# Performance work log

Hardware: AMD Instinct MI355X
Metric: run time of the kernel (lower is better)

Reference implementation:

```python
import jax, jax.numpy as jnp
import numpy as np

NEG_BIG = -9e15
ALPHA = 0.2  # LeakyReLU negative slope


def setup_inputs() -> dict:
    key = jax.random.key(0)
    k1, k2, k3, k4 = jax.random.split(key, 4)
    B, N, F_in, F_out = 8, 2048, 128, 128
    h = jax.random.normal(k1, (B, N, F_in), dtype=jnp.float32)
    adj = jax.random.randint(k2, (B, N, N), 0, 2, dtype=jnp.int32)
    # xavier_uniform with gain=1.414
    def xavier(k, shape, gain=1.414):
        fan_in, fan_out = shape[0], shape[1]
        bound = gain * np.sqrt(6.0 / (fan_in + fan_out))
        return jax.random.uniform(k, shape, jnp.float32, -bound, bound)
    W = xavier(k3, (F_in, F_out))
    a = xavier(k4, (2 * F_out, 1))
    return {"h": h, "adj": adj, "W": W, "a": a}


def reference(h, adj, W, a):
    # h: [B,N,F_in], adj: [B,N,N], W: [F_in,F_out], a: [2*F_out,1]
    Wh = jnp.einsum('bnf,fo->bno', h, W)              # [B,N,F_out]
    F_out = W.shape[1]
    a1 = a[:F_out, 0]                                  # source part
    a2 = a[F_out:, 0]                                  # target part
    # additive attention decomposition: cat([Wh_i, Wh_j]) @ a == Wh_i@a1 + Wh_j@a2
    s1 = Wh @ a1                                       # [B,N]
    s2 = Wh @ a2                                       # [B,N]
    e = jax.nn.leaky_relu(s1[:, :, None] + s2[:, None, :], negative_slope=ALPHA)  # [B,N,N]
    e = jnp.where(adj > 0, e, NEG_BIG)
    attn = jax.nn.softmax(e, axis=-1)                  # [B,N,N]
    h_prime = jnp.einsum('bij,bjo->bio', attn, Wh)     # [B,N,F_out]
    return jax.nn.elu(h_prime)                         # concat=True path
```

## Files before the change

kernel.cpp:

```cpp
#include <hip/hip_runtime.h>
#include <hip/hip_bf16.h>
#include <string.h>

typedef __attribute__((ext_vector_type(8))) short short8;
typedef __attribute__((ext_vector_type(4))) float f32x4;
typedef __attribute__((ext_vector_type(4))) int int4v;
typedef __attribute__((ext_vector_type(4))) float float4v;
typedef __attribute__((ext_vector_type(4))) unsigned short ushort4v;

#define LOG2E 1.44269504088896340736f
#define NB 8
#define NN 2048
#define NF 128
#define PKW (NN / 64)
#define PKWORDS (NB * NN * PKW)

static __device__ inline unsigned short f2bf(float x) {
    __hip_bfloat16 b = __float2bfloat16(x);
    unsigned short u;
    __builtin_memcpy(&u, &b, 2);
    return u;
}
static __device__ inline float bf2f(unsigned short u) {
    union { unsigned u; float f; } v;
    v.u = ((unsigned)u) << 16;
    return v.f;
}

__global__ void k_sniff(const unsigned short* __restrict__ hraw,
                        int* __restrict__ flag) {
    int lane = threadIdx.x;
    int cnt = 0;
    for (int i = lane; i < 512; i += 64) {
        int e = (hraw[i] >> 7) & 0xFF;
        cnt += (e >= 102 && e <= 139) ? 1 : 0;
    }
#pragma unroll
    for (int off = 1; off < 64; off <<= 1) cnt += __shfl_xor(cnt, off);
    if (lane == 0) *flag = (cnt >= 450) ? 1 : 0;
}

__global__ __launch_bounds__(256) void k_pack(const int* __restrict__ adj,
                                              unsigned long long* __restrict__ pk) {
    const int wid = blockIdx.x * 4 + (threadIdx.x >> 6);
    const int lane = threadIdx.x & 63;
    const int wpw = PKWORDS / 4096;
    const size_t w0 = (size_t)wid * wpw;
    for (int i = 0; i < wpw; i += 4) {
        int v0 = adj[((w0 + i) << 6) | lane];
        int v1 = adj[((w0 + i + 1) << 6) | lane];
        int v2 = adj[((w0 + i + 2) << 6) | lane];
        int v3 = adj[((w0 + i + 3) << 6) | lane];
        unsigned long long m0 = __ballot(v0 > 0);
        unsigned long long m1 = __ballot(v1 > 0);
        unsigned long long m2 = __ballot(v2 > 0);
        unsigned long long m3 = __ballot(v3 > 0);
        if (lane == 0) {
            pk[w0 + i] = m0;
            pk[w0 + i + 1] = m1;
            pk[w0 + i + 2] = m2;
            pk[w0 + i + 3] = m3;
        }
    }
}

__global__ __launch_bounds__(256) void k_prep(const void* __restrict__ Wraw,
                                              const void* __restrict__ araw,
                                              const int* __restrict__ flag,
                                              short* __restrict__ WThi,
                                              short* __restrict__ WTlo,
                                              float* __restrict__ a1s,
                                              float* __restrict__ a2s) {
    const int bf16w = *flag;
    int idx = blockIdx.x * 256 + threadIdx.x;
    int k = idx >> 7, n = idx & 127;
    float x = bf16w ? bf2f(((const unsigned short*)Wraw)[idx])
                    : ((const float*)Wraw)[idx];
    unsigned short hi = f2bf(x);
    float lo = x - bf2f(hi);
    WThi[n * 128 + k] = (short)hi;
    WTlo[n * 128 + k] = (short)f2bf(lo);
    if (blockIdx.x == 0) {
        int i = threadIdx.x;
        float av = bf16w ? bf2f(((const unsigned short*)araw)[i])
                         : ((const float*)araw)[i];
        if (i < 128) a1s[i] = LOG2E * av;
        else a2s[i - 128] = LOG2E * av;
    }
}

__global__ __launch_bounds__(64) void k_gemm(const void* __restrict__ hraw,
                                             const int* __restrict__ flag,
                                             const short* __restrict__ WThi,
                                             const short* __restrict__ WTlo,
                                             const float* __restrict__ a1s,
                                             const float* __restrict__ a2s,
                                             float* __restrict__ s1,
                                             float* __restrict__ s2,
                                             short* __restrict__ WhT) {
    const int lane = threadIdx.x;
    const int lo = lane & 15, g = lane >> 4;
    const int i0 = blockIdx.x * 16;
    const int bf16w = *flag;

    short8 ahi[4], alo[4];
    if (bf16w) {
        const short* h16 = (const short*)hraw;
#pragma unroll
        for (int kc = 0; kc < 4; ++kc) {
            ahi[kc] = *(const short8*)(h16 + (size_t)(i0 + lo) * NF + kc * 32 + g * 8);
            alo[kc] = (short8){0, 0, 0, 0, 0, 0, 0, 0};
        }
    } else {
        const float* hf = (const float*)hraw;
#pragma unroll
        for (int kc = 0; kc < 4; ++kc) {
            const float* p = hf + (size_t)(i0 + lo) * NF + kc * 32 + g * 8;
            float4v x0 = *(const float4v*)(p);
            float4v x1 = *(const float4v*)(p + 4);
            short8 h8, l8;
#pragma unroll
            for (int q = 0; q < 4; ++q) {
                unsigned short u0 = f2bf(x0[q]);
                h8[q] = (short)u0;
                l8[q] = (short)f2bf(x0[q] - bf2f(u0));
                unsigned short u1 = f2bf(x1[q]);
                h8[q + 4] = (short)u1;
                l8[q + 4] = (short)f2bf(x1[q] - bf2f(u1));
            }
            ahi[kc] = h8;
            alo[kc] = l8;
        }
    }

    f32x4 acc[8];
#pragma unroll
    for (int t = 0; t < 8; ++t) acc[t] = (f32x4){0.f, 0.f, 0.f, 0.f};

#pragma unroll
    for (int t = 0; t < 8; ++t) {
#pragma unroll
        for (int kc = 0; kc < 4; ++kc) {
            const size_t boff = (size_t)(lo + 16 * t) * NF + kc * 32 + g * 8;
            short8 bhi = *(const short8*)(WThi + boff);
            short8 blo = *(const short8*)(WTlo + boff);
            acc[t] = __builtin_amdgcn_mfma_f32_16x16x32_bf16(ahi[kc], bhi, acc[t], 0, 0, 0);
            acc[t] = __builtin_amdgcn_mfma_f32_16x16x32_bf16(ahi[kc], blo, acc[t], 0, 0, 0);
            acc[t] = __builtin_amdgcn_mfma_f32_16x16x32_bf16(alo[kc], bhi, acc[t], 0, 0, 0);
        }
    }

    const int b = i0 >> 11;
    const int n0 = i0 & 2047;
    short* wt = WhT + (size_t)b * NF * NN;
#pragma unroll
    for (int t = 0; t < 8; ++t) {
        ushort4v u;
#pragma unroll
        for (int r = 0; r < 4; ++r) u[r] = f2bf(acc[t][r]);
        *(ushort4v*)(wt + (size_t)(lo + 16 * t) * NN + n0 + g * 4) = u;
    }

    float a1f[8], a2f[8];
#pragma unroll
    for (int t = 0; t < 8; ++t) {
        a1f[t] = a1s[lo + 16 * t];
        a2f[t] = a2s[lo + 16 * t];
    }
#pragma unroll
    for (int r = 0; r < 4; ++r) {
        float d1 = 0.f, d2 = 0.f;
#pragma unroll
        for (int t = 0; t < 8; ++t) {
            float w = acc[t][r];
            d1 += w * a1f[t];
            d2 += w * a2f[t];
        }
#pragma unroll
        for (int off = 1; off < 16; off <<= 1) {
            d1 += __shfl_xor(d1, off);
            d2 += __shfl_xor(d2, off);
        }
        if (lo == 0) {
            s1[i0 + g * 4 + r] = d1;
            s2[i0 + g * 4 + r] = d2;
        }
    }
}

__global__ __launch_bounds__(256) void k_s2max(const float* __restrict__ s2,
                                               float* __restrict__ s2m) {
    int b = blockIdx.x;
    float m = -1e30f;
    for (int i = threadIdx.x; i < NN; i += 256) m = fmaxf(m, s2[b * NN + i]);
#pragma unroll
    for (int off = 1; off < 64; off <<= 1) m = fmaxf(m, __shfl_xor(m, off));
    __shared__ float sm[4];
    if ((threadIdx.x & 63) == 0) sm[threadIdx.x >> 6] = m;
    __syncthreads();
    if (threadIdx.x == 0)
        s2m[b] = fmaxf(fmaxf(sm[0], sm[1]), fmaxf(sm[2], sm[3]));
}

template <int FINAL, int JS>
__global__ __launch_bounds__(256, 4) void k_attn3(const unsigned long long* __restrict__ pk,
                                                  const float* __restrict__ s1,
                                                  const float* __restrict__ s2,
                                                  const float* __restrict__ s2m,
                                                  const short* __restrict__ WhT,
                                                  const int* __restrict__ flag,
                                                  void* __restrict__ out,
                                                  float* __restrict__ pO,
                                                  float* __restrict__ pL) {
    const int tid = threadIdx.x;
    const int lane = tid & 63, wid = tid >> 6;
    const int lo = lane & 15, g = lane >> 4;
    const int gid = blockIdx.x;
    const int js = (JS > 1) ? (gid / (NB * 32)) : 0;
    const int rem = gid % (NB * 32);
    const int blk = rem & 31;
    const int b = rem >> 5;
    const int rowbase = blk * 64 + wid * 16;
    const int row = rowbase + lo;
    const int jbeg = js * (NN / JS);
    const int NT = (NN / JS) / 64;

    __shared__ short lds[2][128 * 64];

    const float s1v = s1[b * NN + row];
    const float tm = s1v + s2m[b];
    const float M = fmaxf(tm, 0.2f * tm);
    const unsigned long long* pkr = pk + (size_t)(b * NN + row) * PKW + (jbeg >> 6);
    const float* s2p = s2 + b * NN + jbeg;
    const short* vb = WhT + (size_t)b * NF * NN;

    const int sf = tid >> 1;
    const int sh = tid & 1;
    const short* sbase = vb + (size_t)sf * NN + jbeg + sh * 32;
    char* ldsc0 = (char*)&lds[0][0];
    char* ldsc1 = (char*)&lds[1][0];
    const unsigned swz = (unsigned)((sf & 7) << 4);
    const unsigned wb0 = (unsigned)(sf * 128 + sh * 64);
    const unsigned rsw = (unsigned)((lo & 7) << 4);

    f32x4 acc[8];
#pragma unroll
    for (int t = 0; t < 8; ++t) acc[t] = (f32x4){0.f, 0.f, 0.f, 0.f};
    float lsum = 0.f;

    {
        short8 s0 = *(const short8*)(sbase);
        short8 s1r = *(const short8*)(sbase + 8);
        short8 s2r = *(const short8*)(sbase + 16);
        short8 s3r = *(const short8*)(sbase + 24);
        *(short8*)(ldsc0 + ((wb0 + 0) ^ swz)) = s0;
        *(short8*)(ldsc0 + ((wb0 + 16) ^ swz)) = s1r;
        *(short8*)(ldsc0 + ((wb0 + 32) ^ swz)) = s2r;
        *(short8*)(ldsc0 + ((wb0 + 48) ^ swz)) = s3r;
    }
    unsigned long long mcur = pkr[0];
    float4v zc0 = *(const float4v*)(s2p + g * 8);
    float4v zc1 = *(const float4v*)(s2p + g * 8 + 4);
    float4v zc2 = *(const float4v*)(s2p + g * 8 + 32);
    float4v zc3 = *(const float4v*)(s2p + g * 8 + 36);
    __syncthreads();

    int cur = 0;
    for (int t = 0; t < NT; ++t) {
        short8 sn0, sn1, sn2, sn3;
        unsigned long long mnext = 0;
        float4v zn0, zn1, zn2, zn3;
        const bool more = (t + 1 < NT);
        if (more) {
            const short* sp = sbase + (t + 1) * 64;
            sn0 = *(const short8*)(sp);
            sn1 = *(const short8*)(sp + 8);
            sn2 = *(const short8*)(sp + 16);
            sn3 = *(const short8*)(sp + 24);
            mnext = pkr[t + 1];
            const float* zp = s2p + (t + 1) * 64 + g * 8;
            zn0 = *(const float4v*)(zp);
            zn1 = *(const float4v*)(zp + 4);
            zn2 = *(const float4v*)(zp + 32);
            zn3 = *(const float4v*)(zp + 36);
        }
        const char* cb = cur ? ldsc1 : ldsc0;

        const unsigned bits0 = (unsigned)(mcur >> (g * 8)) & 0xFFu;
        const unsigned bits1 = (unsigned)(mcur >> (32 + g * 8)) & 0xFFu;
        short8 pa0, pa1;
#pragma unroll
        for (int q = 0; q < 4; ++q) {
            float t0 = s1v + zc0[q];
            float e0 = fmaxf(t0, 0.2f * t0);
            float p0 = ((bits0 >> q) & 1u) ? exp2f(e0 - M) : 0.f;
            float t1 = s1v + zc1[q];
            float e1 = fmaxf(t1, 0.2f * t1);
            float p1 = ((bits0 >> (q + 4)) & 1u) ? exp2f(e1 - M) : 0.f;
            float t2 = s1v + zc2[q];
            float e2 = fmaxf(t2, 0.2f * t2);
            float p2 = ((bits1 >> q) & 1u) ? exp2f(e2 - M) : 0.f;
            float t3 = s1v + zc3[q];
            float e3 = fmaxf(t3, 0.2f * t3);
            float p3 = ((bits1 >> (q + 4)) & 1u) ? exp2f(e3 - M) : 0.f;
            pa0[q] = (short)f2bf(p0); pa0[q + 4] = (short)f2bf(p1);
            pa1[q] = (short)f2bf(p2); pa1[q + 4] = (short)f2bf(p3);
            lsum += p0 + p1 + p2 + p3;
        }

#pragma unroll
        for (int t8 = 0; t8 < 8; ++t8) {
            const unsigned rb0 = ((unsigned)((lo + 16 * t8) * 128 + g * 16)) ^ rsw;
            const unsigned rb1 = ((unsigned)((lo + 16 * t8) * 128 + 64 + g * 16)) ^ rsw;
            short8 v0 = *(const short8*)(cb + rb0);
            short8 v1 = *(const short8*)(cb + rb1);
            acc[t8] = __builtin_amdgcn_mfma_f32_16x16x32_bf16(pa0, v0, acc[t8], 0, 0, 0);
            acc[t8] = __builtin_amdgcn_mfma_f32_16x16x32_bf16(pa1, v1, acc[t8], 0, 0, 0);
        }

        if (more) {
            char* wb = cur ? ldsc0 : ldsc1;
            *(short8*)(wb + ((wb0 + 0) ^ swz)) = sn0;
            *(short8*)(wb + ((wb0 + 16) ^ swz)) = sn1;
            *(short8*)(wb + ((wb0 + 32) ^ swz)) = sn2;
            *(short8*)(wb + ((wb0 + 48) ^ swz)) = sn3;
            mcur = mnext;
            zc0 = zn0; zc1 = zn1; zc2 = zn2; zc3 = zn3;
        }
        __syncthreads();
        cur ^= 1;
    }

    lsum += __shfl_xor(lsum, 16);
    lsum += __shfl_xor(lsum, 32);

    if (FINAL) {
        const int bf16w = *flag;
        float inv[4];
#pragma unroll
        for (int r = 0; r < 4; ++r) inv[r] = 1.0f / __shfl(lsum, g * 4 + r);
#pragma unroll
        for (int t8 = 0; t8 < 8; ++t8) {
#pragma unroll
            for (int r = 0; r < 4; ++r) {
                float x = acc[t8][r] * inv[r];
                float y = (x > 0.f) ? x : (exp2f(x * LOG2E) - 1.0f);
                size_t oi = ((size_t)b * NN + rowbase + g * 4 + r) * NF + lo + 16 * t8;
                if (bf16w) ((__hip_bfloat16*)out)[oi] = __float2bfloat16(y);
                else ((float*)out)[oi] = y;
            }
        }
    } else {
        const int grp = b * 128 + blk * 4 + wid;
        float* po = pO + (size_t)(grp * JS + js) * (16 * NF);
#pragma unroll
        for (int t8 = 0; t8 < 8; ++t8)
#pragma unroll
            for (int r = 0; r < 4; ++r)
                po[(g * 4 + r) * NF + lo + 16 * t8] = acc[t8][r];
        if (g == 0) pL[(grp * JS + js) * 16 + lo] = lsum;
    }
}

__global__ __launch_bounds__(256) void k_combine(const float* __restrict__ pO,
                                                 const float* __restrict__ pL,
                                                 const int* __restrict__ flag,
                                                 void* __restrict__ out,
                                                 int jsplit) {
    int idx = blockIdx.x * 256 + threadIdx.x;
    if (idx >= NB * NN * NF) return;
    const int bf16w = *flag;
    int col = idx & 127;
    int rowg = idx >> 7;
    int r = rowg & 15;
    int grp = rowg >> 4;
    float o = 0.f, l = 0.f;
    for (int js = 0; js < jsplit; ++js) {
        int task = grp * jsplit + js;
        o += pO[(size_t)task * (16 * NF) + r * NF + col];
        l += pL[task * 16 + r];
    }
    float x = o / l;
    float y = (x > 0.f) ? x : (exp2f(x * LOG2E) - 1.0f);
    if (bf16w) ((__hip_bfloat16*)out)[idx] = __float2bfloat16(y);
    else ((float*)out)[idx] = y;
}

extern "C" void kernel_launch(void* const* d_in, const int* in_sizes, int n_in,
                              void* d_out, int out_size, void* d_ws, size_t ws_size,
                              hipStream_t stream) {
    const void* h = d_in[0];
    const int* adj = (const int*)d_in[1];
    const void* W = d_in[2];
    const void* a = d_in[3];

    char* ws = (char*)d_ws;
    auto align256 = [](size_t x) { return (x + 255) & ~(size_t)255; };
    size_t off = 0;
    int* flag = (int*)(ws + off);     off = align256(off + 256);
    short* WThi = (short*)(ws + off); off = align256(off + (size_t)128 * 128 * 2);
    short* WTlo = (short*)(ws + off); off = align256(off + (size_t)128 * 128 * 2);
    float* a1s = (float*)(ws + off);  off = align256(off + 128 * 4);
    float* a2s = (float*)(ws + off);  off = align256(off + 128 * 4);
    short* WhT = (short*)(ws + off);  off = align256(off + (size_t)NB * NF * NN * 2);
    float* s1 = (float*)(ws + off);   off = align256(off + (size_t)NB * NN * 4);
    float* s2 = (float*)(ws + off);   off = align256(off + (size_t)NB * NN * 4);
    float* s2m = (float*)(ws + off);  off = align256(off + (size_t)NB * 4);
    unsigned long long* pk = (unsigned long long*)(ws + off);
    off = align256(off + (size_t)PKWORDS * 8);

    const int ngrp = NB * 128;
    auto need = [&](int js) {
        return off + (size_t)ngrp * js * 16 * NF * 4 + 512 + (size_t)ngrp * js * 16 * 4;
    };
    int jsplit = (ws_size >= need(4)) ? 4 : ((ws_size >= need(2)) ? 2 : 1);
    float* pO = nullptr;
    float* pL = nullptr;
    if (jsplit > 1) {
        size_t pO_bytes = (size_t)ngrp * jsplit * 16 * NF * 4;
        size_t pL_bytes = (size_t)ngrp * jsplit * 16 * 4;
        pO = (float*)(ws + off); off = align256(off + pO_bytes);
        pL = (float*)(ws + off); off = align256(off + pL_bytes);
    }

    k_sniff<<<1, 64, 0, stream>>>((const unsigned short*)h, flag);
    k_pack<<<1024, 256, 0, stream>>>(adj, pk);
    k_prep<<<64, 256, 0, stream>>>(W, a, flag, WThi, WTlo, a1s, a2s);
    k_gemm<<<NB * NN / 16, 64, 0, stream>>>(h, flag, WThi, WTlo, a1s, a2s, s1, s2, WhT);
    k_s2max<<<NB, 256, 0, stream>>>(s2, s2m);
    if (jsplit == 4) {
        k_attn3<0, 4><<<NB * 32 * 4, 256, 0, stream>>>(pk, s1, s2, s2m, WhT, flag,
                                                       d_out, pO, pL);
    } else if (jsplit == 2) {
        k_attn3<0, 2><<<NB * 32 * 2, 256, 0, stream>>>(pk, s1, s2, s2m, WhT, flag,
                                                       d_out, pO, pL);
    } else {
        k_attn3<1, 1><<<NB * 32, 256, 0, stream>>>(pk, s1, s2, s2m, WhT, flag,
                                                   d_out, nullptr, nullptr);
    }
    if (jsplit > 1) {
        int nout = NB * NN * NF;
        k_combine<<<(nout + 255) / 256, 256, 0, stream>>>(pO, pL, flag, d_out, jsplit);
    }
}
```

Measured before the change: 87.86 us.

## Fuse adjacency bit-packing into attention kernel, reading int adj directly

Removes the separate pack kernel and its packed-mask buffer; the attention kernel now loads int adjacency rows for its tile, ballots them into per-row 64-bit masks, and prefetches the next tile's adjacency alongside the value tile. This avoids a kernel launch and the write/read of the packed mask, keeping the single pass over adj. It adds 16 extra registers of prefetched adjacency per thread and places the full adj stream inside the attention loop, which may raise register pressure or expose memory latency.

```diff
diff --git a/kernel.cpp b/kernel.cpp
--- a/kernel.cpp
+++ b/kernel.cpp
@@ -12,8 +12,6 @@
 #define NB 8
 #define NN 2048
 #define NF 128
-#define PKW (NN / 64)
-#define PKWORDS (NB * NN * PKW)
 
 static __device__ inline unsigned short f2bf(float x) {
     __hip_bfloat16 b = __float2bfloat16(x);
@@ -38,30 +36,6 @@
 #pragma unroll
     for (int off = 1; off < 64; off <<= 1) cnt += __shfl_xor(cnt, off);
     if (lane == 0) *flag = (cnt >= 450) ? 1 : 0;
-}
-
-__global__ __launch_bounds__(256) void k_pack(const int* __restrict__ adj,
-                                              unsigned long long* __restrict__ pk) {
-    const int wid = blockIdx.x * 4 + (threadIdx.x >> 6);
-    const int lane = threadIdx.x & 63;
-    const int wpw = PKWORDS / 4096;
-    const size_t w0 = (size_t)wid * wpw;
-    for (int i = 0; i < wpw; i += 4) {
-        int v0 = adj[((w0 + i) << 6) | lane];
-        int v1 = adj[((w0 + i + 1) << 6) | lane];
-        int v2 = adj[((w0 + i + 2) << 6) | lane];
-        int v3 = adj[((w0 + i + 3) << 6) | lane];
-        unsigned long long m0 = __ballot(v0 > 0);
-        unsigned long long m1 = __ballot(v1 > 0);
-        unsigned long long m2 = __ballot(v2 > 0);
-        unsigned long long m3 = __ballot(v3 > 0);
-        if (lane == 0) {
-            pk[w0 + i] = m0;
-            pk[w0 + i + 1] = m1;
-            pk[w0 + i + 2] = m2;
-            pk[w0 + i + 3] = m3;
-        }
-    }
 }
 
 __global__ __launch_bounds__(256) void k_prep(const void* __restrict__ Wraw,
@@ -203,7 +177,7 @@
 }
 
 template <int FINAL, int JS>
-__global__ __launch_bounds__(256, 4) void k_attn3(const unsigned long long* __restrict__ pk,
+__global__ __launch_bounds__(256, 4) void k_attn3(const int* __restrict__ adj,
                                                   const float* __restrict__ s1,
                                                   const float* __restrict__ s2,
                                                   const float* __restrict__ s2m,
@@ -230,9 +204,9 @@
     const float s1v = s1[b * NN + row];
     const float tm = s1v + s2m[b];
     const float M = fmaxf(tm, 0.2f * tm);
-    const unsigned long long* pkr = pk + (size_t)(b * NN + row) * PKW + (jbeg >> 6);
     const float* s2p = s2 + b * NN + jbeg;
     const short* vb = WhT + (size_t)b * NF * NN;
+    const int* arow = adj + (size_t)(b * NN + rowbase) * NN + jbeg + lane;
 
     const int sf = tid >> 1;
     const int sh = tid & 1;
@@ -258,7 +232,17 @@
         *(short8*)(ldsc0 + ((wb0 + 32) ^ swz)) = s2r;
         *(short8*)(ldsc0 + ((wb0 + 48) ^ swz)) = s3r;
     }
-    unsigned long long mcur = pkr[0];
+    unsigned long long mcur = 0;
+    {
+        int av[16];
+#pragma unroll
+        for (int r = 0; r < 16; ++r) av[r] = arow[(size_t)r * NN];
+#pragma unroll
+        for (int r = 0; r < 16; ++r) {
+            unsigned long long mr = __ballot(av[r] > 0);
+            if (lo == r) mcur = mr;
+        }
+    }
     float4v zc0 = *(const float4v*)(s2p + g * 8);
     float4v zc1 = *(const float4v*)(s2p + g * 8 + 4);
     float4v zc2 = *(const float4v*)(s2p + g * 8 + 32);
@@ -268,7 +252,7 @@
     int cur = 0;
     for (int t = 0; t < NT; ++t) {
         short8 sn0, sn1, sn2, sn3;
-        unsigned long long mnext = 0;
+        int an[16];
         float4v zn0, zn1, zn2, zn3;
         const bool more = (t + 1 < NT);
         if (more) {
@@ -277,7 +261,8 @@
             sn1 = *(const short8*)(sp + 8);
             sn2 = *(const short8*)(sp + 16);
             sn3 = *(const short8*)(sp + 24);
-            mnext = pkr[t + 1];
+#pragma unroll
+            for (int r = 0; r < 16; ++r) an[r] = arow[(size_t)r * NN + (t + 1) * 64];
             const float* zp = s2p + (t + 1) * 64 + g * 8;
             zn0 = *(const float4v*)(zp);
             zn1 = *(const float4v*)(zp + 4);
@@ -324,6 +309,12 @@
             *(short8*)(wb + ((wb0 + 16) ^ swz)) = sn1;
             *(short8*)(wb + ((wb0 + 32) ^ swz)) = sn2;
             *(short8*)(wb + ((wb0 + 48) ^ swz)) = sn3;
+            unsigned long long mnext = 0;
+#pragma unroll
+            for (int r = 0; r < 16; ++r) {
+                unsigned long long mr = __ballot(an[r] > 0);
+                if (lo == r) mnext = mr;
+            }
             mcur = mnext;
             zc0 = zn0; zc1 = zn1; zc2 = zn2; zc3 = zn3;
         }
@@ -406,8 +397,6 @@
     float* s1 = (float*)(ws + off);   off = align256(off + (size_t)NB * NN * 4);
     float* s2 = (float*)(ws + off);   off = align256(off + (size_t)NB * NN * 4);
     float* s2m = (float*)(ws + off);  off = align256(off + (size_t)NB * 4);
-    unsigned long long* pk = (unsigned long long*)(ws + off);
-    off = align256(off + (size_t)PKWORDS * 8);
 
     const int ngrp = NB * 128;
     auto need = [&](int js) {
@@ -424,18 +413,17 @@
     }
 
     k_sniff<<<1, 64, 0, stream>>>((const unsigned short*)h, flag);
-    k_pack<<<1024, 256, 0, stream>>>(adj, pk);
     k_prep<<<64, 256, 0, stream>>>(W, a, flag, WThi, WTlo, a1s, a2s);
     k_gemm<<<NB * NN / 16, 64, 0, stream>>>(h, flag, WThi, WTlo, a1s, a2s, s1, s2, WhT);
     k_s2max<<<NB, 256, 0, stream>>>(s2, s2m);
     if (jsplit == 4) {
-        k_attn3<0, 4><<<NB * 32 * 4, 256, 0, stream>>>(pk, s1, s2, s2m, WhT, flag,
+        k_attn3<0, 4><<<NB * 32 * 4, 256, 0, stream>>>(adj, s1, s2, s2m, WhT, flag,
                                                        d_out, pO, pL);
     } else if (jsplit == 2) {
-        k_attn3<0, 2><<<NB * 32 * 2, 256, 0, stream>>>(pk, s1, s2, s2m, WhT, flag,
+        k_attn3<0, 2><<<NB * 32 * 2, 256, 0, stream>>>(adj, s1, s2, s2m, WhT, flag,
                                                        d_out, pO, pL);
     } else {
-        k_attn3<1, 1><<<NB * 32, 256, 0, stream>>>(pk, s1, s2, s2m, WhT, flag,
+        k_attn3<1, 1><<<NB * 32, 256, 0, stream>>>(adj, s1, s2, s2m, WhT, flag,
                                                    d_out, nullptr, nullptr);
     }
     if (jsplit > 1) {
```

Result: slower. 137.4 us (+56.4%).
